# Performance work log

Hardware: AMD Instinct MI355X
Metric: run time of the kernel (lower is better)

## Reference

```python
import jax, jax.numpy as jnp
import numpy as np

B, S, E, H = 4, 8192, 512, 8
D = E // H  # head_dim = 64


def setup_inputs() -> dict:
    key = jax.random.key(0)
    ks = jax.random.split(key, 9)
    scale = 1.0 / np.sqrt(E)
    x = jax.random.normal(ks[0], (B, S, E), dtype=jnp.float32)
    # torch nn.Linear convention: y = x @ W.T + b, W has shape (out, in)
    Wp = jax.random.uniform(ks[1], (E, E), jnp.float32, -scale, scale)
    bp = jax.random.uniform(ks[2], (E,), jnp.float32, -scale, scale)
    Wc = jax.random.uniform(ks[3], (E, E), jnp.float32, -scale, scale)
    bc = jax.random.uniform(ks[4], (E,), jnp.float32, -scale, scale)
    Ws = jax.random.uniform(ks[5], (E, E), jnp.float32, -scale, scale)
    bs = jax.random.uniform(ks[6], (E,), jnp.float32, -scale, scale)
    Wo = jax.random.uniform(ks[7], (E, E), jnp.float32, -scale, scale)
    bo = jax.random.uniform(ks[8], (E,), jnp.float32, -scale, scale)
    return {"x": x, "Wp": Wp, "bp": bp, "Wc": Wc, "bc": bc,
            "Ws": Ws, "bs": bs, "Wo": Wo, "bo": bo}


def reference(x, Wp, bp, Wc, bc, Ws, bs, Wo, bo):
    # Faithful to TreeAttention.forward with tree_structure=None (default path).
    # NOTE: original views projections as (B,S,H,D) without transposing head/seq,
    # so the matmuls mix HEADS per token (HxH scores), not tokens.
    b, s, _ = x.shape
    parent = (jnp.einsum('bse,fe->bsf', x, Wp) + bp).reshape(b, s, H, D)
    child = (jnp.einsum('bse,fe->bsf', x, Wc) + bc).reshape(b, s, H, D)
    sibling = (jnp.einsum('bse,fe->bsf', x, Ws) + bs).reshape(b, s, H, D)
    # per-token head-mixing scores: (B, S, H, H)
    scores = jnp.einsum('bshd,bstd->bsht', parent, child) / jnp.sqrt(
        jnp.asarray(D, dtype=x.dtype))
    attention = jax.nn.softmax(scores, axis=-1)
    # dropout is identity in eval mode (reference runs in inference mode)
    out = jnp.einsum('bsht,bstd->bshd', attention, sibling).reshape(b, s, E)
    return jnp.einsum('bse,fe->bsf', out, Wo) + bo
```

## Files before the change

kernel.cpp:

```cpp
#include <hip/hip_runtime.h>
#include <hip/hip_bf16.h>

typedef unsigned short u16;
typedef __attribute__((ext_vector_type(8))) short bf16x8;
typedef __attribute__((ext_vector_type(4))) float f32x4;
typedef __attribute__((ext_vector_type(8))) unsigned short u16x8;

#define GLDS(gp, lp) __builtin_amdgcn_global_load_lds( \
    (const __attribute__((address_space(1))) void*)(gp), \
    (__attribute__((address_space(3))) void*)(lp), 16, 0, 0)

__device__ __forceinline__ u16 f2b(float f) {
  unsigned u = __builtin_bit_cast(unsigned, f);
  return (u16)((u + 0x7fffu + ((u >> 16) & 1u)) >> 16);
}
__device__ __forceinline__ float b2f(u16 s) {
  return __builtin_bit_cast(float, (unsigned)s << 16);
}

#define BARX() do { __builtin_amdgcn_sched_barrier(0); \
  asm volatile("s_barrier" ::: "memory"); \
  __builtin_amdgcn_sched_barrier(0); } while (0)

__global__ __launch_bounds__(256) void convert_k(
    const float* __restrict__ x, const float* __restrict__ Wp,
    const float* __restrict__ Wc, const float* __restrict__ Ws,
    const float* __restrict__ Wo, u16* __restrict__ xb,
    u16* __restrict__ wall, u16* __restrict__ wob)
{
  const long CX = 2097152;
  const long CW = 98304;
  const long CO = 32768;
  const long total = CX + CW + CO;
  for (long i = (long)blockIdx.x * blockDim.x + threadIdx.x; i < total;
       i += (long)gridDim.x * blockDim.x) {
    const float* src; u16* dst;
    if (i < CX) {
      src = x + i * 8; dst = xb + i * 8;
    } else if (i < CX + CW) {
      long e = (i - CX) * 8;
      int n = (int)(e >> 9), k = (int)(e & 511);
      const float* wr = (n < 512)  ? (Wp + (long)n * 512)
                      : (n < 1024) ? (Wc + (long)(n - 512) * 512)
                                   : (Ws + (long)(n - 1024) * 512);
      src = wr + k; dst = wall + e;
    } else {
      long e = (i - CX - CW) * 8; src = Wo + e; dst = wob + e;
    }
    f32x4 v0 = *(const f32x4*)src;
    f32x4 v1 = *(const f32x4*)(src + 4);
    u16x8 o;
    o[0]=f2b(v0[0]); o[1]=f2b(v0[1]); o[2]=f2b(v0[2]); o[3]=f2b(v0[3]);
    o[4]=f2b(v1[0]); o[5]=f2b(v1[1]); o[6]=f2b(v1[2]); o[7]=f2b(v1[3]);
    *(u16x8*)dst = o;
  }
}

template<int NC, bool BF16OUT>
__global__ __launch_bounds__(512, 2) void gemm8(
    const u16* __restrict__ A, const u16* __restrict__ Bw,
    const float* __restrict__ bias0, const float* __restrict__ bias1,
    const float* __restrict__ bias2, void* __restrict__ Cout)
{
  __shared__ alignas(16) char smem[131072];
  char* sAc = smem;
  char* sBc = smem + 65536;

  const int tid = threadIdx.x;
  const int w = tid >> 6, lane = tid & 63;
  const int wr = w >> 2, wc = w & 3;
  const int ln15 = lane & 15, g4 = lane >> 4, l7 = lane & 7;

  const int nbx = NC / 256;
  const int nwg = nbx * 128;
  const int qq = nwg / 8;
  const int flat = blockIdx.x;
  const int swz = (flat & 7) * qq + (flat >> 3);
  const int bx = swz % nbx, by = swz / nbx;
  const long row0 = (long)by * 256;
  const int col0 = bx * 256;

  const int gsw = (tid & 7) ^ ((tid >> 3) & 7);
  const u16* pA = A + (row0 + (tid >> 3)) * 512 + gsw * 8;
  const u16* pB = Bw + ((long)col0 + (tid >> 3)) * 512 + gsw * 8;

#define STAGE(pp, tt) do { \
    const u16* a0_ = pA + (tt) * 64; const u16* b0_ = pB + (tt) * 64; \
    char* da_ = sAc + (pp) * 32768 + w * 1024; \
    char* db_ = sBc + (pp) * 32768 + w * 1024; \
    GLDS(a0_, da_);          GLDS(a0_ + 32768, da_ + 8192); \
    GLDS(a0_ + 65536, da_ + 16384); GLDS(a0_ + 98304, da_ + 24576); \
    GLDS(b0_, db_);          GLDS(b0_ + 32768, db_ + 8192); \
    GLDS(b0_ + 65536, db_ + 16384); GLDS(b0_ + 98304, db_ + 24576); \
  } while (0)

  const int gkb0 = ((0 + g4) ^ l7) * 16;
  const int gkb1 = ((4 + g4) ^ l7) * 16;
  const int arow = (wr * 128 + ln15) * 128;
  const int brow = (wc * 64 + ln15) * 128;

#define LOAD_A(MH) do { \
    _Pragma("unroll") for (int mf = 0; mf < 4; ++mf) { \
      aF[mf][0] = *(const bf16x8*)(bufA + (MH) * 8192 + mf * 2048 + gkb0); \
      aF[mf][1] = *(const bf16x8*)(bufA + (MH) * 8192 + mf * 2048 + gkb1); \
    } } while (0)
#define LOAD_B(NH, BF) do { \
    _Pragma("unroll") for (int nf = 0; nf < 2; ++nf) { \
      BF[nf][0] = *(const bf16x8*)(bufB + (NH) * 4096 + nf * 2048 + gkb0); \
      BF[nf][1] = *(const bf16x8*)(bufB + (NH) * 4096 + nf * 2048 + gkb1); \
    } } while (0)
#define MFMA_Q(MH, NH, BF) do { \
    _Pragma("unroll") for (int mf = 0; mf < 4; ++mf) \
    _Pragma("unroll") for (int nf = 0; nf < 2; ++nf) { \
      f32x4 c_ = acc[(MH) * 4 + mf][(NH) * 2 + nf]; \
      c_ = __builtin_amdgcn_mfma_f32_16x16x32_bf16(aF[mf][0], BF[nf][0], c_, 0, 0, 0); \
      c_ = __builtin_amdgcn_mfma_f32_16x16x32_bf16(aF[mf][1], BF[nf][1], c_, 0, 0, 0); \
      acc[(MH) * 4 + mf][(NH) * 2 + nf] = c_; \
    } } while (0)

  f32x4 acc[8][4] = {};

  STAGE(0, 0);
  asm volatile("s_waitcnt vmcnt(0)" ::: "memory");
  BARX();

  for (int t = 0; t < 8; ++t) {
    const int p = t & 1;
    const char* bufA = sAc + p * 32768 + arow;
    const char* bufB = sBc + p * 32768 + brow;
    bf16x8 aF[4][2], bFa[2][2], bFb[2][2];

    LOAD_A(0); LOAD_B(0, bFa);
    if (t < 7) STAGE(p ^ 1, t + 1);
    BARX();
    __builtin_amdgcn_s_setprio(1); MFMA_Q(0, 0, bFa); __builtin_amdgcn_s_setprio(0);
    BARX();
    LOAD_B(1, bFb);
    BARX();
    __builtin_amdgcn_s_setprio(1); MFMA_Q(0, 1, bFb); __builtin_amdgcn_s_setprio(0);
    BARX();
    LOAD_A(1);
    BARX();
    __builtin_amdgcn_s_setprio(1); MFMA_Q(1, 1, bFb); __builtin_amdgcn_s_setprio(0);
    BARX();
    __builtin_amdgcn_s_setprio(1); MFMA_Q(1, 0, bFa); __builtin_amdgcn_s_setprio(0);
    if (t < 7) {
      asm volatile("s_waitcnt vmcnt(0)" ::: "memory");
      BARX();
    }
  }

  __syncthreads();
  const long rgb = row0 + wr * 128;
  const int cgb = col0 + wc * 64;
  if (BF16OUT) {
    u16* sc = (u16*)(smem + (w << 14));
#pragma unroll
    for (int n = 0; n < 4; ++n) {
      const int colg = cgb + ln15 + n * 16;
      const float* bp_ = (NC == 512) ? bias0
                         : (colg < 512 ? bias0 : (colg < 1024 ? bias1 : bias2));
      const float bv = bp_[colg & 511];
      const int c = ln15 + n * 16;
      const int gsl = c >> 3, co = c & 7;
#pragma unroll
      for (int mi = 0; mi < 8; ++mi)
#pragma unroll
        for (int j = 0; j < 4; ++j) {
          const int r = mi * 16 + (g4 << 2) + j;
          sc[r * 64 + (((gsl ^ (r & 7)) << 3) | co)] = f2b(acc[mi][n][j] + bv);
        }
    }
    asm volatile("s_waitcnt lgkmcnt(0)" ::: "memory");
    __builtin_amdgcn_sched_barrier(0);
#pragma unroll
    for (int it = 0; it < 16; ++it) {
      const int rr = it * 8 + (lane >> 3);
      const int gl = lane & 7;
      u16x8 v = *(const u16x8*)(sc + rr * 64 + ((gl ^ (rr & 7)) << 3));
      *(u16x8*)((u16*)Cout + (rgb + rr) * NC + cgb + gl * 8) = v;
    }
  } else {
    float* scf = (float*)(smem + (w << 14));
#pragma unroll
    for (int h = 0; h < 2; ++h) {
#pragma unroll
      for (int n = 0; n < 4; ++n) {
        const int colg = cgb + ln15 + n * 16;
        const float bv = bias0[colg & 511];
        const int c = ln15 + n * 16;
        const int gsl = c >> 2, co = c & 3;
#pragma unroll
        for (int mf = 0; mf < 4; ++mf)
#pragma unroll
          for (int j = 0; j < 4; ++j) {
            const int r = mf * 16 + (g4 << 2) + j;
            scf[r * 64 + (((gsl ^ (r & 7)) << 2) | co)] = acc[h * 4 + mf][n][j] + bv;
          }
      }
      asm volatile("s_waitcnt lgkmcnt(0)" ::: "memory");
      __builtin_amdgcn_sched_barrier(0);
#pragma unroll
      for (int it = 0; it < 16; ++it) {
        const int rr = it * 4 + (lane >> 4);
        const int gl = lane & 15;
        f32x4 v = *(const f32x4*)(scf + rr * 64 + ((gl ^ (rr & 7)) << 2));
        *(f32x4*)((float*)Cout + (rgb + h * 64 + rr) * NC + cgb + gl * 4) = v;
      }
      asm volatile("s_waitcnt lgkmcnt(0)" ::: "memory");
      __builtin_amdgcn_sched_barrier(0);
    }
  }
#undef STAGE
#undef LOAD_A
#undef LOAD_B
#undef MFMA_Q
}

__global__ __launch_bounds__(256) void attn_k(const u16* __restrict__ PCS,
                                              u16* __restrict__ OUT)
{
  __shared__ float L[4][1664];
  const int w = threadIdx.x >> 6, lane = threadIdx.x & 63;
  const long token = (long)blockIdx.x * 4 + w;
  float* Lw = L[w];
  const int C0 = 544, S0 = 1088, AT0 = 1600;
  const u16* rowp = PCS + token * 1536;
#pragma unroll
  for (int q = 0; q < 3; ++q) {
    u16x8 v = *(const u16x8*)(rowp + q * 512 + lane * 8);
    float* dst = (q < 2) ? (Lw + q * 544 + (lane >> 3) * 68 + (lane & 7) * 8)
                         : (Lw + S0 + lane * 8);
    f32x4 a = {b2f(v[0]), b2f(v[1]), b2f(v[2]), b2f(v[3])};
    f32x4 b = {b2f(v[4]), b2f(v[5]), b2f(v[6]), b2f(v[7])};
    *(f32x4*)dst = a;
    *(f32x4*)(dst + 4) = b;
  }
  const int h = lane >> 3, t = lane & 7;
  float sc = 0.f;
#pragma unroll
  for (int d = 0; d < 64; d += 4) {
    f32x4 pv = *(const f32x4*)(Lw + h * 68 + d);
    f32x4 cv = *(const f32x4*)(Lw + C0 + t * 68 + d);
    sc += pv[0]*cv[0] + pv[1]*cv[1] + pv[2]*cv[2] + pv[3]*cv[3];
  }
  sc *= 0.125f;
  float mx = sc;
  mx = fmaxf(mx, __shfl_xor(mx, 1));
  mx = fmaxf(mx, __shfl_xor(mx, 2));
  mx = fmaxf(mx, __shfl_xor(mx, 4));
  float e = __expf(sc - mx);
  float sm = e;
  sm += __shfl_xor(sm, 1);
  sm += __shfl_xor(sm, 2);
  sm += __shfl_xor(sm, 4);
  Lw[AT0 + lane] = e / sm;
  float o[8] = {0, 0, 0, 0, 0, 0, 0, 0};
#pragma unroll
  for (int tt = 0; tt < 8; ++tt) {
    const float av = Lw[AT0 + h * 8 + tt];
    f32x4 s0 = *(const f32x4*)(Lw + S0 + tt * 64 + t * 8);
    f32x4 s1 = *(const f32x4*)(Lw + S0 + tt * 64 + t * 8 + 4);
    o[0] += av * s0[0]; o[1] += av * s0[1]; o[2] += av * s0[2]; o[3] += av * s0[3];
    o[4] += av * s1[0]; o[5] += av * s1[1]; o[6] += av * s1[2]; o[7] += av * s1[3];
  }
  u16x8 ov;
#pragma unroll
  for (int j = 0; j < 8; ++j) ov[j] = f2b(o[j]);
  *(u16x8*)(OUT + token * 512 + lane * 8) = ov;
}

extern "C" void kernel_launch(void* const* d_in, const int* in_sizes, int n_in,
                              void* d_out, int out_size, void* d_ws, size_t ws_size,
                              hipStream_t stream) {
  const float* x  = (const float*)d_in[0];
  const float* Wp = (const float*)d_in[1];
  const float* bp = (const float*)d_in[2];
  const float* Wc = (const float*)d_in[3];
  const float* bc = (const float*)d_in[4];
  const float* Ws = (const float*)d_in[5];
  const float* bs = (const float*)d_in[6];
  const float* Wo = (const float*)d_in[7];
  const float* bo = (const float*)d_in[8];

  char* ws = (char*)d_ws;
  u16* xb   = (u16*)ws;
  u16* wall = (u16*)(ws + 33554432);
  u16* wob  = (u16*)(ws + 35127296);
  u16* pcs  = (u16*)(ws + 35651584);
  u16* outb = xb;

  convert_k<<<2048, 256, 0, stream>>>(x, Wp, Wc, Ws, Wo, xb, wall, wob);
  gemm8<1536, true><<<768, 512, 0, stream>>>(xb, wall, bp, bc, bs, pcs);
  attn_k<<<8192, 256, 0, stream>>>(pcs, outb);
  gemm8<512, false><<<256, 512, 0, stream>>>(outb, wob, bo, bo, bo, d_out);
}
```

Measured before the change: 136.1 us.

## Fuse fp32-to-bf16 conversion of x into the QKV GEMM A-tile staging

Removes the separate pass that converted x to bf16 and instead has the first GEMM load fp32 x tiles into registers, convert them, and write bf16 into LDS with the existing swizzle. The conversion kernel now handles only the weights. This removes a full write and re-read of the 32MB bf16 copy of x, but the first GEMM now reads twice as many A bytes, and each A tile is loaded into registers and stored to LDS by hand instead of with direct global-to-LDS loads, which adds register pressure and extra waits.

```diff
diff --git a/kernel.cpp b/kernel.cpp
--- a/kernel.cpp
+++ b/kernel.cpp
@@ -22,43 +22,35 @@
   asm volatile("s_barrier" ::: "memory"); \
   __builtin_amdgcn_sched_barrier(0); } while (0)
 
-__global__ __launch_bounds__(256) void convert_k(
-    const float* __restrict__ x, const float* __restrict__ Wp,
-    const float* __restrict__ Wc, const float* __restrict__ Ws,
-    const float* __restrict__ Wo, u16* __restrict__ xb,
+__global__ __launch_bounds__(256) void convert_w(
+    const float* __restrict__ Wp, const float* __restrict__ Wc,
+    const float* __restrict__ Ws, const float* __restrict__ Wo,
     u16* __restrict__ wall, u16* __restrict__ wob)
 {
-  const long CX = 2097152;
   const long CW = 98304;
-  const long CO = 32768;
-  const long total = CX + CW + CO;
-  for (long i = (long)blockIdx.x * blockDim.x + threadIdx.x; i < total;
-       i += (long)gridDim.x * blockDim.x) {
-    const float* src; u16* dst;
-    if (i < CX) {
-      src = x + i * 8; dst = xb + i * 8;
-    } else if (i < CX + CW) {
-      long e = (i - CX) * 8;
-      int n = (int)(e >> 9), k = (int)(e & 511);
-      const float* wr = (n < 512)  ? (Wp + (long)n * 512)
-                      : (n < 1024) ? (Wc + (long)(n - 512) * 512)
-                                   : (Ws + (long)(n - 1024) * 512);
-      src = wr + k; dst = wall + e;
-    } else {
-      long e = (i - CX - CW) * 8; src = Wo + e; dst = wob + e;
-    }
-    f32x4 v0 = *(const f32x4*)src;
-    f32x4 v1 = *(const f32x4*)(src + 4);
-    u16x8 o;
-    o[0]=f2b(v0[0]); o[1]=f2b(v0[1]); o[2]=f2b(v0[2]); o[3]=f2b(v0[3]);
-    o[4]=f2b(v1[0]); o[5]=f2b(v1[1]); o[6]=f2b(v1[2]); o[7]=f2b(v1[3]);
-    *(u16x8*)dst = o;
-  }
-}
-
-template<int NC, bool BF16OUT>
+  const long i = (long)blockIdx.x * blockDim.x + threadIdx.x;
+  const float* src; u16* dst;
+  if (i < CW) {
+    long e = i * 8;
+    int n = (int)(e >> 9), k = (int)(e & 511);
+    const float* wr = (n < 512)  ? (Wp + (long)n * 512)
+                    : (n < 1024) ? (Wc + (long)(n - 512) * 512)
+                                 : (Ws + (long)(n - 1024) * 512);
+    src = wr + k; dst = wall + e;
+  } else {
+    long e = (i - CW) * 8; src = Wo + e; dst = wob + e;
+  }
+  f32x4 v0 = *(const f32x4*)src;
+  f32x4 v1 = *(const f32x4*)(src + 4);
+  u16x8 o;
+  o[0]=f2b(v0[0]); o[1]=f2b(v0[1]); o[2]=f2b(v0[2]); o[3]=f2b(v0[3]);
+  o[4]=f2b(v1[0]); o[5]=f2b(v1[1]); o[6]=f2b(v1[2]); o[7]=f2b(v1[3]);
+  *(u16x8*)dst = o;
+}
+
+template<int NC, bool BF16OUT, bool AF32>
 __global__ __launch_bounds__(512, 2) void gemm8(
-    const u16* __restrict__ A, const u16* __restrict__ Bw,
+    const void* __restrict__ Ain, const u16* __restrict__ Bw,
     const float* __restrict__ bias0, const float* __restrict__ bias1,
     const float* __restrict__ bias2, void* __restrict__ Cout)
 {
@@ -81,18 +73,38 @@
   const int col0 = bx * 256;
 
   const int gsw = (tid & 7) ^ ((tid >> 3) & 7);
-  const u16* pA = A + (row0 + (tid >> 3)) * 512 + gsw * 8;
+  const float* pX = (const float*)Ain + (row0 + (tid >> 3)) * 512 + (tid & 7) * 8;
+  const u16* pA = (const u16*)Ain + (row0 + (tid >> 3)) * 512 + gsw * 8;
   const u16* pB = Bw + ((long)col0 + (tid >> 3)) * 512 + gsw * 8;
-
-#define STAGE(pp, tt) do { \
-    const u16* a0_ = pA + (tt) * 64; const u16* b0_ = pB + (tt) * 64; \
+  const int aw_dst = (tid >> 3) * 128 + gsw * 16;
+
+#define STAGE_A(pp, tt) do { \
+    const u16* a0_ = pA + (tt) * 64; \
     char* da_ = sAc + (pp) * 32768 + w * 1024; \
-    char* db_ = sBc + (pp) * 32768 + w * 1024; \
     GLDS(a0_, da_);          GLDS(a0_ + 32768, da_ + 8192); \
     GLDS(a0_ + 65536, da_ + 16384); GLDS(a0_ + 98304, da_ + 24576); \
+  } while (0)
+#define STAGE_B(pp, tt) do { \
+    const u16* b0_ = pB + (tt) * 64; \
+    char* db_ = sBc + (pp) * 32768 + w * 1024; \
     GLDS(b0_, db_);          GLDS(b0_ + 32768, db_ + 8192); \
     GLDS(b0_ + 65536, db_ + 16384); GLDS(b0_ + 98304, db_ + 24576); \
   } while (0)
+#define A_ISSUE(tt) do { \
+    const float* ax_ = pX + (tt) * 64; \
+    _Pragma("unroll") for (int j = 0; j < 4; ++j) { \
+      av[j][0] = *(const f32x4*)(ax_ + j * 32768); \
+      av[j][1] = *(const f32x4*)(ax_ + j * 32768 + 4); \
+    } } while (0)
+#define A_WRITE(pp) do { \
+    _Pragma("unroll") for (int j = 0; j < 4; ++j) { \
+      u16x8 o_; \
+      _Pragma("unroll") for (int e = 0; e < 4; ++e) { \
+        o_[e]     = __builtin_bit_cast(u16, __float2bfloat16(av[j][0][e])); \
+        o_[e + 4] = __builtin_bit_cast(u16, __float2bfloat16(av[j][1][e])); \
+      } \
+      *(u16x8*)(sAc + (pp) * 32768 + j * 8192 + aw_dst) = o_; \
+    } } while (0)
 
   const int gkb0 = ((0 + g4) ^ l7) * 16;
   const int gkb1 = ((4 + g4) ^ l7) * 16;
@@ -119,9 +131,17 @@
     } } while (0)
 
   f32x4 acc[8][4] = {};
-
-  STAGE(0, 0);
-  asm volatile("s_waitcnt vmcnt(0)" ::: "memory");
+  f32x4 av[4][2];
+
+  if constexpr (AF32) { A_ISSUE(0); } else { STAGE_A(0, 0); }
+  STAGE_B(0, 0);
+  if constexpr (AF32) {
+    A_WRITE(0);
+    asm volatile("s_waitcnt vmcnt(0)" ::: "memory");
+    asm volatile("s_waitcnt lgkmcnt(0)" ::: "memory");
+  } else {
+    asm volatile("s_waitcnt vmcnt(0)" ::: "memory");
+  }
   BARX();
 
   for (int t = 0; t < 8; ++t) {
@@ -131,7 +151,10 @@
     bf16x8 aF[4][2], bFa[2][2], bFb[2][2];
 
     LOAD_A(0); LOAD_B(0, bFa);
-    if (t < 7) STAGE(p ^ 1, t + 1);
+    if (t < 7) {
+      if constexpr (AF32) { A_ISSUE(t + 1); } else { STAGE_A(p ^ 1, t + 1); }
+      STAGE_B(p ^ 1, t + 1);
+    }
     BARX();
     __builtin_amdgcn_s_setprio(1); MFMA_Q(0, 0, bFa); __builtin_amdgcn_s_setprio(0);
     BARX();
@@ -145,7 +168,13 @@
     BARX();
     __builtin_amdgcn_s_setprio(1); MFMA_Q(1, 0, bFa); __builtin_amdgcn_s_setprio(0);
     if (t < 7) {
-      asm volatile("s_waitcnt vmcnt(0)" ::: "memory");
+      if constexpr (AF32) {
+        A_WRITE(p ^ 1);
+        asm volatile("s_waitcnt vmcnt(0)" ::: "memory");
+        asm volatile("s_waitcnt lgkmcnt(0)" ::: "memory");
+      } else {
+        asm volatile("s_waitcnt vmcnt(0)" ::: "memory");
+      }
       BARX();
     }
   }
@@ -211,7 +240,10 @@
       __builtin_amdgcn_sched_barrier(0);
     }
   }
-#undef STAGE
+#undef STAGE_A
+#undef STAGE_B
+#undef A_ISSUE
+#undef A_WRITE
 #undef LOAD_A
 #undef LOAD_B
 #undef MFMA_Q
@@ -284,14 +316,13 @@
   const float* bo = (const float*)d_in[8];
 
   char* ws = (char*)d_ws;
-  u16* xb   = (u16*)ws;
-  u16* wall = (u16*)(ws + 33554432);
-  u16* wob  = (u16*)(ws + 35127296);
-  u16* pcs  = (u16*)(ws + 35651584);
-  u16* outb = xb;
-
-  convert_k<<<2048, 256, 0, stream>>>(x, Wp, Wc, Ws, Wo, xb, wall, wob);
-  gemm8<1536, true><<<768, 512, 0, stream>>>(xb, wall, bp, bc, bs, pcs);
+  u16* wall = (u16*)ws;
+  u16* wob  = (u16*)(ws + 1572864);
+  u16* pcs  = (u16*)(ws + 2097152);
+  u16* outb = (u16*)(ws + 102760448);
+
+  convert_w<<<512, 256, 0, stream>>>(Wp, Wc, Ws, Wo, wall, wob);
+  gemm8<1536, true, true><<<768, 512, 0, stream>>>(x, wall, bp, bc, bs, pcs);
   attn_k<<<8192, 256, 0, stream>>>(pcs, outb);
-  gemm8<512, false><<<256, 512, 0, stream>>>(outb, wob, bo, bo, bo, d_out);
-}
+  gemm8<512, false, false><<<256, 512, 0, stream>>>(outb, wob, bo, bo, bo, d_out);
+}
```

After: 140.8 us. 3.5% more time.
